# Kernel optimization log

Measured on AMD Instinct MI355X. Metric: run time of the kernel, lower is better.

## Reference

```python
import jax, jax.numpy as jnp
import numpy as np

B, N, K = 8, 16384, 32
EPS = 1e-5


def setup_inputs() -> dict:
    key = jax.random.key(0)
    ks = jax.random.split(key, 11)
    xyz = jax.random.normal(ks[0], (B, N, 3), jnp.float32)
    intensity = jax.random.normal(ks[1], (B, 3, N), jnp.float32)
    indices = jax.random.randint(ks[2], (B, N, K), 0, N)
    # linear_p: Conv2d(3,3,1)+BN+ReLU, then Conv2d(3,1,1)
    w1 = jax.random.normal(ks[3], (3, 3), jnp.float32) * 0.3
    b1 = jax.random.normal(ks[4], (3,), jnp.float32) * 0.1
    gamma = jax.random.uniform(ks[5], (3,), jnp.float32, 0.5, 1.5)
    beta = jax.random.normal(ks[6], (3,), jnp.float32) * 0.1
    mean = jax.random.normal(ks[7], (3,), jnp.float32) * 0.1
    var = jax.random.uniform(ks[8], (3,), jnp.float32, 0.5, 1.5)
    w2 = jax.random.normal(ks[9], (1, 3), jnp.float32) * 0.3
    b2 = jax.random.normal(ks[10], (1,), jnp.float32) * 0.1
    return dict(xyz=xyz, intensity=intensity, indices=indices, w1=w1, b1=b1,
                gamma=gamma, beta=beta, mean=mean, var=var, w2=w2, b2=b2)


def reference(xyz, intensity, indices, w1, b1, gamma, beta, mean, var, w2, b2):
    # neighbor gathers (irregular access)
    xyz_nb = jax.vmap(lambda p, i: p[i])(xyz, indices)          # [B,N,K,3]
    i_nb = jax.vmap(lambda ft, i: ft[:, i])(intensity, indices)  # [B,3,N,K]
    # relative position + gaussian kernel
    pos = xyz_nb - xyz[:, :, None, :]                            # [B,N,K,3]
    pos_g = jnp.exp(-2.0 * pos * pos)
    pos_g = jnp.transpose(pos_g, (0, 3, 1, 2))                   # [B,3,N,K]
    # 1x1 conv (3->3) + eval-mode BN + ReLU
    h = jnp.einsum('oc,bcnk->bonk', w1, pos_g) + b1[None, :, None, None]
    scale = gamma / jnp.sqrt(var + EPS)
    h = (h - mean[None, :, None, None]) * scale[None, :, None, None] + beta[None, :, None, None]
    h = jax.nn.relu(h)
    # 1x1 conv (3->1), softmax over neighbors
    w = jnp.einsum('oc,bcnk->bonk', w2, h) + b2[None, :, None, None]  # [B,1,N,K]
    w = jax.nn.softmax(w, axis=-1)
    # weighted reduce over neighbors
    return jnp.sum(i_nb * w, axis=-1)                            # [B,3,N]
```

## Files before the change

### kernel.cpp

```cpp
#include <hip/hip_runtime.h>
#include <hip/hip_fp16.h>
#include <math.h>

#define PB 8
#define PN 16384
#define PK 32
#define PEPS 1e-5f

__device__ __forceinline__ uint2 pack3(float a, float b, float c) {
    union { __half2 h2[2]; uint2 u; } r;
    r.h2[0] = __halves2half2(__float2half_rn(a), __float2half_rn(b));
    r.h2[1] = __halves2half2(__float2half_rn(c), __float2half_rn(0.f));
    return r.u;
}

__device__ __forceinline__ float pair_add(float v) {
    int t = __builtin_amdgcn_update_dpp(0, __float_as_int(v), 0xB1, 0xf, 0xf, true);
    return v + __int_as_float(t);
}

__global__ __launch_bounds__(1024, 4) void sa_fused(
    const float* __restrict__ xyz,
    const float* __restrict__ intensity,
    const int*   __restrict__ indices,
    const float* __restrict__ w1, const float* __restrict__ b1,
    const float* __restrict__ gamma_, const float* __restrict__ beta_,
    const float* __restrict__ mean_, const float* __restrict__ var_,
    const float* __restrict__ w2, const float* __restrict__ b2,
    float* __restrict__ out)
{
    __shared__ uint4 sbuf[PN / 2];
    const uint2* sx = (const uint2*)sbuf;

    const int tid   = threadIdx.x;
    const int b     = blockIdx.x & 7;
    const int chunk = blockIdx.x >> 3;
    const int n     = chunk * 512 + (tid >> 1);
    const int q     = (b << 14) + n;
    const int half  = tid & 1;

    const float sc0 = gamma_[0] * rsqrtf(var_[0] + PEPS);
    const float sc1 = gamma_[1] * rsqrtf(var_[1] + PEPS);
    const float sc2 = gamma_[2] * rsqrtf(var_[2] + PEPS);
    const float A00 = w1[0] * sc0, A01 = w1[1] * sc0, A02 = w1[2] * sc0;
    const float A10 = w1[3] * sc1, A11 = w1[4] * sc1, A12 = w1[5] * sc1;
    const float A20 = w1[6] * sc2, A21 = w1[7] * sc2, A22 = w1[8] * sc2;
    const float d0 = (b1[0] - mean_[0]) * sc0 + beta_[0];
    const float d1 = (b1[1] - mean_[1]) * sc1 + beta_[1];
    const float d2 = (b1[2] - mean_[2]) * sc2 + beta_[2];
    const float w0 = w2[0], w1v = w2[1], w2v = w2[2];
    const float bias2 = b2[0];

    const float cx = xyz[3 * (size_t)q + 0];
    const float cy = xyz[3 * (size_t)q + 1];
    const float cz = xyz[3 * (size_t)q + 2];

    int idxs[16];
    {
        const int4* ip = (const int4*)(indices + (size_t)q * PK + half * 16);
#pragma unroll
        for (int j = 0; j < 4; ++j) {
            const int4 v = ip[j];
            idxs[4 * j + 0] = v.x; idxs[4 * j + 1] = v.y;
            idxs[4 * j + 2] = v.z; idxs[4 * j + 3] = v.w;
        }
    }

    {
        const float4* xv = (const float4*)(xyz + (size_t)b * PN * 3);
#pragma unroll
        for (int j = 0; j < 4; ++j) {
            const int m = tid + j * 1024;
            const float4 f0 = xv[3 * m + 0];
            const float4 f1 = xv[3 * m + 1];
            const float4 f2 = xv[3 * m + 2];
            union { uint2 u2[4]; uint4 u4[2]; } pk;
            pk.u2[0] = pack3(f0.x, f0.y, f0.z);
            pk.u2[1] = pack3(f0.w, f1.x, f1.y);
            pk.u2[2] = pack3(f1.z, f1.w, f2.x);
            pk.u2[3] = pack3(f2.y, f2.z, f2.w);
            sbuf[2 * m + 0] = pk.u4[0];
            sbuf[2 * m + 1] = pk.u4[1];
        }
    }
    __syncthreads();

    float ev[16];
    float s = 0.f;
#pragma unroll
    for (int k = 0; k < 16; ++k) {
        const uint2 xz = sx[idxs[k]];
        const float2 nxy = __half22float2(*(const __half2*)&xz.x);
        const float  nz  = __half2float(*(const __half*)&xz.y);

        const float px = nxy.x - cx;
        const float py = nxy.y - cy;
        const float pz = nz - cz;

        const float g0 = __expf(-2.f * px * px);
        const float g1 = __expf(-2.f * py * py);
        const float g2 = __expf(-2.f * pz * pz);

        float h0 = fmaf(A00, g0, fmaf(A01, g1, fmaf(A02, g2, d0)));
        float h1 = fmaf(A10, g0, fmaf(A11, g1, fmaf(A12, g2, d1)));
        float h2 = fmaf(A20, g0, fmaf(A21, g1, fmaf(A22, g2, d2)));
        h0 = fmaxf(h0, 0.f); h1 = fmaxf(h1, 0.f); h2 = fmaxf(h2, 0.f);
        const float logit = fmaf(w0, h0, fmaf(w1v, h1, fmaf(w2v, h2, bias2)));

        const float e = __expf(logit);
        ev[k] = e;
        s += e;
    }

    __syncthreads();

    {
        const float4* iv = (const float4*)(intensity + (size_t)b * 3 * PN);
#pragma unroll
        for (int j = 0; j < 4; ++j) {
            const int m = tid + j * 1024;
            const float4 f0 = iv[m];
            const float4 f1 = iv[4096 + m];
            const float4 f2 = iv[8192 + m];
            union { uint2 u2[4]; uint4 u4[2]; } pk;
            pk.u2[0] = pack3(f0.x, f1.x, f2.x);
            pk.u2[1] = pack3(f0.y, f1.y, f2.y);
            pk.u2[2] = pack3(f0.z, f1.z, f2.z);
            pk.u2[3] = pack3(f0.w, f1.w, f2.w);
            sbuf[2 * m + 0] = pk.u4[0];
            sbuf[2 * m + 1] = pk.u4[1];
        }
    }
    __syncthreads();

    float a0 = 0.f, a1 = 0.f, a2 = 0.f;
#pragma unroll
    for (int k = 0; k < 16; ++k) {
        const uint2 it = sx[idxs[k]];
        const float2 i01 = __half22float2(*(const __half2*)&it.x);
        const float  i2v = __half2float(*(const __half*)&it.y);
        const float e = ev[k];
        a0 = fmaf(e, i01.x, a0);
        a1 = fmaf(e, i01.y, a1);
        a2 = fmaf(e, i2v,  a2);
    }

    s  = pair_add(s);
    a0 = pair_add(a0);
    a1 = pair_add(a1);
    a2 = pair_add(a2);

    if (half == 0) {
        const float inv = 1.f / s;
        float* ob = out + (size_t)b * 3 * PN;
        ob[0 * PN + n] = a0 * inv;
        ob[1 * PN + n] = a1 * inv;
        ob[2 * PN + n] = a2 * inv;
    }
}

extern "C" void kernel_launch(void* const* d_in, const int* in_sizes, int n_in,
                              void* d_out, int out_size, void* d_ws, size_t ws_size,
                              hipStream_t stream) {
    const float* xyz       = (const float*)d_in[0];
    const float* intensity = (const float*)d_in[1];
    const int*   indices   = (const int*)d_in[2];
    const float* w1        = (const float*)d_in[3];
    const float* b1        = (const float*)d_in[4];
    const float* gamma_    = (const float*)d_in[5];
    const float* beta_     = (const float*)d_in[6];
    const float* mean_     = (const float*)d_in[7];
    const float* var_      = (const float*)d_in[8];
    const float* w2        = (const float*)d_in[9];
    const float* b2        = (const float*)d_in[10];
    float* out = (float*)d_out;

    const int points = PB * PN;
    sa_fused<<<(points * 2) / 1024, 1024, 0, stream>>>(xyz, intensity, indices,
                                                       w1, b1, gamma_, beta_,
                                                       mean_, var_, w2, b2, out);
}
```

Measured before the change: 102.2 us.

## Pre-pack fp16 point tables once and stream into LDS via global_load_lds

Adds a separate pack kernel that converts xyz and intensity to packed fp16 tables in workspace once per call. The main kernel then fills shared memory with direct global-to-LDS async loads instead of having all 256 blocks per batch redo the fp32 load, convert and store work. The xyz table load is issued before the index loads so the two overlap. The cost is an extra kernel launch and a round trip through workspace memory, and the old fused kernel is kept as a fallback when the workspace is too small.

```diff
diff --git a/kernel.cpp b/kernel.cpp
--- a/kernel.cpp
+++ b/kernel.cpp
@@ -7,21 +7,47 @@
 #define PK 32
 #define PEPS 1e-5f
 
-__device__ __forceinline__ uint2 pack3(float a, float b, float c) {
-    union { __half2 h2[2]; uint2 u; } r;
-    r.h2[0] = __halves2half2(__float2half_rn(a), __float2half_rn(b));
-    r.h2[1] = __halves2half2(__float2half_rn(c), __float2half_rn(0.f));
-    return r.u;
-}
-
 __device__ __forceinline__ float pair_add(float v) {
     int t = __builtin_amdgcn_update_dpp(0, __float_as_int(v), 0xB1, 0xf, 0xf, true);
     return v + __int_as_float(t);
 }
 
-__global__ __launch_bounds__(1024, 4) void sa_fused(
+__device__ __forceinline__ void gload_lds16(const uint4* g, void* l) {
+    __builtin_amdgcn_global_load_lds(
+        (const __attribute__((address_space(1))) uint32_t*)g,
+        (__attribute__((address_space(3))) uint32_t*)l, 16, 0, 0);
+}
+
+__global__ __launch_bounds__(256) void sa_pack(
     const float* __restrict__ xyz,
     const float* __restrict__ intensity,
+    uint2* __restrict__ pxyz,
+    uint2* __restrict__ pint)
+{
+    const int t = blockIdx.x * 256 + threadIdx.x;
+    const int b = t >> 14;
+    const int n = t & (PN - 1);
+    const float x = xyz[(long)t * 3 + 0];
+    const float y = xyz[(long)t * 3 + 1];
+    const float z = xyz[(long)t * 3 + 2];
+    const float* ib = intensity + (long)b * 3 * PN;
+    const float i0 = ib[0 * PN + n];
+    const float i1 = ib[1 * PN + n];
+    const float i2 = ib[2 * PN + n];
+
+    union { __half2 h2[2]; uint2 u; } rx, ri;
+    rx.h2[0] = __halves2half2(__float2half_rn(x), __float2half_rn(y));
+    rx.h2[1] = __halves2half2(__float2half_rn(z), __float2half_rn(0.f));
+    ri.h2[0] = __halves2half2(__float2half_rn(i0), __float2half_rn(i1));
+    ri.h2[1] = __halves2half2(__float2half_rn(i2), __float2half_rn(0.f));
+    pxyz[t] = rx.u;
+    pint[t] = ri.u;
+}
+
+__global__ __launch_bounds__(1024, 4) void sa_main(
+    const uint2* __restrict__ pxyz,
+    const uint2* __restrict__ pint,
+    const float* __restrict__ xyz,
     const int*   __restrict__ indices,
     const float* __restrict__ w1, const float* __restrict__ b1,
     const float* __restrict__ gamma_, const float* __restrict__ beta_,
@@ -38,6 +64,8 @@
     const int n     = chunk * 512 + (tid >> 1);
     const int q     = (b << 14) + n;
     const int half  = tid & 1;
+
+    const int wavebase = (tid >> 6) << 8;
 
     const float sc0 = gamma_[0] * rsqrtf(var_[0] + PEPS);
     const float sc1 = gamma_[1] * rsqrtf(var_[1] + PEPS);
@@ -55,6 +83,14 @@
     const float cy = xyz[3 * (size_t)q + 1];
     const float cz = xyz[3 * (size_t)q + 2];
 
+    {
+        const uint4* gsrc = (const uint4*)(pxyz + ((size_t)b << 14));
+        uint32_t* lbase = (uint32_t*)sbuf;
+#pragma unroll
+        for (int j = 0; j < 8; ++j)
+            gload_lds16(gsrc + j * 1024 + tid, lbase + j * 4096 + wavebase);
+    }
+
     int idxs[16];
     {
         const int4* ip = (const int4*)(indices + (size_t)q * PK + half * 16);
@@ -65,7 +101,122 @@
             idxs[4 * j + 2] = v.z; idxs[4 * j + 3] = v.w;
         }
     }
-
+    __syncthreads();
+
+    float ev[16];
+    float s = 0.f;
+#pragma unroll
+    for (int k = 0; k < 16; ++k) {
+        const uint2 xz = sx[idxs[k]];
+        const float2 nxy = __half22float2(*(const __half2*)&xz.x);
+        const float  nz  = __half2float(*(const __half*)&xz.y);
+
+        const float px = nxy.x - cx;
+        const float py = nxy.y - cy;
+        const float pz = nz - cz;
+
+        const float g0 = __expf(-2.f * px * px);
+        const float g1 = __expf(-2.f * py * py);
+        const float g2 = __expf(-2.f * pz * pz);
+
+        float h0 = fmaf(A00, g0, fmaf(A01, g1, fmaf(A02, g2, d0)));
+        float h1 = fmaf(A10, g0, fmaf(A11, g1, fmaf(A12, g2, d1)));
+        float h2 = fmaf(A20, g0, fmaf(A21, g1, fmaf(A22, g2, d2)));
+        h0 = fmaxf(h0, 0.f); h1 = fmaxf(h1, 0.f); h2 = fmaxf(h2, 0.f);
+        const float logit = fmaf(w0, h0, fmaf(w1v, h1, fmaf(w2v, h2, bias2)));
+
+        const float e = __expf(logit);
+        ev[k] = e;
+        s += e;
+    }
+
+    __syncthreads();
+
+    {
+        const uint4* gsrc = (const uint4*)(pint + ((size_t)b << 14));
+        uint32_t* lbase = (uint32_t*)sbuf;
+#pragma unroll
+        for (int j = 0; j < 8; ++j)
+            gload_lds16(gsrc + j * 1024 + tid, lbase + j * 4096 + wavebase);
+    }
+    __syncthreads();
+
+    float a0 = 0.f, a1 = 0.f, a2 = 0.f;
+#pragma unroll
+    for (int k = 0; k < 16; ++k) {
+        const uint2 it = sx[idxs[k]];
+        const float2 i01 = __half22float2(*(const __half2*)&it.x);
+        const float  i2v = __half2float(*(const __half*)&it.y);
+        const float e = ev[k];
+        a0 = fmaf(e, i01.x, a0);
+        a1 = fmaf(e, i01.y, a1);
+        a2 = fmaf(e, i2v,  a2);
+    }
+
+    s  = pair_add(s);
+    a0 = pair_add(a0);
+    a1 = pair_add(a1);
+    a2 = pair_add(a2);
+
+    if (half == 0) {
+        const float inv = 1.f / s;
+        float* ob = out + (size_t)b * 3 * PN;
+        ob[0 * PN + n] = a0 * inv;
+        ob[1 * PN + n] = a1 * inv;
+        ob[2 * PN + n] = a2 * inv;
+    }
+}
+
+__device__ __forceinline__ uint2 pack3(float a, float b, float c) {
+    union { __half2 h2[2]; uint2 u; } r;
+    r.h2[0] = __halves2half2(__float2half_rn(a), __float2half_rn(b));
+    r.h2[1] = __halves2half2(__float2half_rn(c), __float2half_rn(0.f));
+    return r.u;
+}
+__global__ __launch_bounds__(1024, 4) void sa_fallback(
+    const float* __restrict__ xyz, const float* __restrict__ intensity,
+    const int* __restrict__ indices,
+    const float* __restrict__ w1, const float* __restrict__ b1,
+    const float* __restrict__ gamma_, const float* __restrict__ beta_,
+    const float* __restrict__ mean_, const float* __restrict__ var_,
+    const float* __restrict__ w2, const float* __restrict__ b2,
+    float* __restrict__ out)
+{
+    __shared__ uint4 sbuf[PN / 2];
+    const uint2* sx = (const uint2*)sbuf;
+    const int tid   = threadIdx.x;
+    const int b     = blockIdx.x & 7;
+    const int chunk = blockIdx.x >> 3;
+    const int n     = chunk * 512 + (tid >> 1);
+    const int q     = (b << 14) + n;
+    const int half  = tid & 1;
+
+    const float sc0 = gamma_[0] * rsqrtf(var_[0] + PEPS);
+    const float sc1 = gamma_[1] * rsqrtf(var_[1] + PEPS);
+    const float sc2 = gamma_[2] * rsqrtf(var_[2] + PEPS);
+    const float A00 = w1[0] * sc0, A01 = w1[1] * sc0, A02 = w1[2] * sc0;
+    const float A10 = w1[3] * sc1, A11 = w1[4] * sc1, A12 = w1[5] * sc1;
+    const float A20 = w1[6] * sc2, A21 = w1[7] * sc2, A22 = w1[8] * sc2;
+    const float d0 = (b1[0] - mean_[0]) * sc0 + beta_[0];
+    const float d1 = (b1[1] - mean_[1]) * sc1 + beta_[1];
+    const float d2 = (b1[2] - mean_[2]) * sc2 + beta_[2];
+    const float w0 = w2[0], w1v = w2[1], w2v = w2[2];
+    const float bias2 = b2[0];
+
+    const float cx = xyz[3 * (size_t)q + 0];
+    const float cy = xyz[3 * (size_t)q + 1];
+    const float cz = xyz[3 * (size_t)q + 2];
+
+    int idxs[16];
+    {
+        const int4* ip = (const int4*)(indices + (size_t)q * PK + half * 16);
+#pragma unroll
+        for (int j = 0; j < 4; ++j) {
+            const int4 v = ip[j];
+            idxs[4 * j + 0] = v.x; idxs[4 * j + 1] = v.y;
+            idxs[4 * j + 2] = v.z; idxs[4 * j + 3] = v.w;
+        }
+    }
     {
         const float4* xv = (const float4*)(xyz + (size_t)b * PN * 3);
 #pragma unroll
@@ -85,35 +236,25 @@
     }
     __syncthreads();
 
-    float ev[16];
-    float s = 0.f;
+    float ev[16]; float s = 0.f;
 #pragma unroll
     for (int k = 0; k < 16; ++k) {
         const uint2 xz = sx[idxs[k]];
         const float2 nxy = __half22float2(*(const __half2*)&xz.x);
         const float  nz  = __half2float(*(const __half*)&xz.y);
-
-        const float px = nxy.x - cx;
-        const float py = nxy.y - cy;
-        const float pz = nz - cz;
-
+        const float px = nxy.x - cx, py = nxy.y - cy, pz = nz - cz;
         const float g0 = __expf(-2.f * px * px);
         const float g1 = __expf(-2.f * py * py);
         const float g2 = __expf(-2.f * pz * pz);
-
         float h0 = fmaf(A00, g0, fmaf(A01, g1, fmaf(A02, g2, d0)));
         float h1 = fmaf(A10, g0, fmaf(A11, g1, fmaf(A12, g2, d1)));
         float h2 = fmaf(A20, g0, fmaf(A21, g1, fmaf(A22, g2, d2)));
         h0 = fmaxf(h0, 0.f); h1 = fmaxf(h1, 0.f); h2 = fmaxf(h2, 0.f);
         const float logit = fmaf(w0, h0, fmaf(w1v, h1, fmaf(w2v, h2, bias2)));
-
         const float e = __expf(logit);
-        ev[k] = e;
-        s += e;
-    }
-
-    __syncthreads();
-
+        ev[k] = e; s += e;
+    }
+    __syncthreads();
     {
         const float4* iv = (const float4*)(intensity + (size_t)b * 3 * PN);
 #pragma unroll
@@ -132,7 +273,6 @@
         }
     }
     __syncthreads();
-
     float a0 = 0.f, a1 = 0.f, a2 = 0.f;
 #pragma unroll
     for (int k = 0; k < 16; ++k) {
@@ -144,12 +284,7 @@
         a1 = fmaf(e, i01.y, a1);
         a2 = fmaf(e, i2v,  a2);
     }
-
-    s  = pair_add(s);
-    a0 = pair_add(a0);
-    a1 = pair_add(a1);
-    a2 = pair_add(a2);
-
+    s = pair_add(s); a0 = pair_add(a0); a1 = pair_add(a1); a2 = pair_add(a2);
     if (half == 0) {
         const float inv = 1.f / s;
         float* ob = out + (size_t)b * 3 * PN;
@@ -176,7 +311,18 @@
     float* out = (float*)d_out;
 
     const int points = PB * PN;
-    sa_fused<<<(points * 2) / 1024, 1024, 0, stream>>>(xyz, intensity, indices,
-                                                       w1, b1, gamma_, beta_,
-                                                       mean_, var_, w2, b2, out);
-}
+    const size_t arr_bytes = (size_t)points * 8;
+
+    if (ws_size >= 2 * arr_bytes) {
+        uint2* pxyz = (uint2*)d_ws;
+        uint2* pint = (uint2*)((char*)d_ws + arr_bytes);
+        sa_pack<<<points / 256, 256, 0, stream>>>(xyz, intensity, pxyz, pint);
+        sa_main<<<(points * 2) / 1024, 1024, 0, stream>>>(
+            pxyz, pint, xyz, indices, w1, b1, gamma_, beta_, mean_, var_,
+            w2, b2, out);
+    } else {
+        sa_fallback<<<(points * 2) / 1024, 1024, 0, stream>>>(
+            xyz, intensity, indices, w1, b1, gamma_, beta_, mean_, var_,
+            w2, b2, out);
+    }
+}
```

Result: no change. 103.6 us (+1.3%).
